# Kernel optimization log

Measured on AMD Instinct MI355X. Metric: run time of the kernel, lower is better.

Reference implementation:

```python
import jax, jax.numpy as jnp
import numpy as np

B, T, D, H = 2, 2048, 1024, 16
HD = D // H  # head_dim = 64


def setup_inputs() -> dict:
    key = jax.random.key(0)
    ks = jax.random.split(key, 5)
    s = 0.02
    return {
        "x": jax.random.normal(ks[0], (B, T, D), dtype=jnp.float32),
        "Wqkv": jax.random.normal(ks[1], (3 * D, D), dtype=jnp.float32) * s,
        "bqkv": jax.random.normal(ks[2], (3 * D,), dtype=jnp.float32) * s,
        "Wproj": jax.random.normal(ks[3], (D, D), dtype=jnp.float32) * s,
        "bproj": jax.random.normal(ks[4], (D,), dtype=jnp.float32) * s,
    }


def reference(x, Wqkv, bqkv, Wproj, bproj):
    b, t, d = x.shape
    qkv = x @ Wqkv.T + bqkv                      # [B,T,3D]
    q, k, v = jnp.split(qkv, 3, axis=-1)
    # [B,T,D] -> [B,H,T,HD]
    def to_heads(u):
        return u.reshape(b, t, H, HD).transpose(0, 2, 1, 3)
    q, k, v = to_heads(q), to_heads(k), to_heads(v)
    scale = 1.0 / jnp.sqrt(jnp.float32(HD))
    attn = jnp.einsum("bhqd,bhkd->bhqk", q, k) * scale   # [B,H,T,T]
    causal = jnp.tril(jnp.ones((t, t), dtype=bool))
    attn = jnp.where(causal[None, None, :, :], attn, -jnp.inf)
    attn = jax.nn.softmax(attn, axis=-1)
    scores = jnp.einsum("bhqk,bhkd->bhqd", attn, v)       # [B,H,T,HD]
    scores = scores.transpose(0, 2, 1, 3).reshape(b, t, d)
    return scores @ Wproj.T + bproj
```

## Files before the change

### kernel.cpp

```cpp
#include <hip/hip_runtime.h>

typedef __bf16 bf16_8 __attribute__((ext_vector_type(8)));
typedef __bf16 bf16_4 __attribute__((ext_vector_type(4)));
typedef __bf16 bf16_2 __attribute__((ext_vector_type(2)));
typedef float  f32_4  __attribute__((ext_vector_type(4)));
typedef float  f32_16 __attribute__((ext_vector_type(16)));

typedef __attribute__((address_space(1))) const void* as1_cvp;
typedef __attribute__((address_space(3))) void*       as3_vp;

__device__ __forceinline__ void load16_to_lds(const void* g, void* l) {
    __builtin_amdgcn_global_load_lds((as1_cvp)g, (as3_vp)l, 16, 0, 0);
}

__device__ __forceinline__ float fast_exp2(float x) {
#if __has_builtin(__builtin_amdgcn_exp2f)
    return __builtin_amdgcn_exp2f(x);
#else
    return exp2f(x);
#endif
}

__device__ __forceinline__ unsigned pk2(float lo, float hi) {
    union { bf16_2 h; unsigned u; } t;
    t.h = bf16_2{(__bf16)lo, (__bf16)hi};
    return t.u;
}

__device__ __forceinline__ void pswap(unsigned &a, unsigned &b) {
    asm("v_permlane32_swap_b32 %0, %1" : "+v"(a), "+v"(b));
}

__global__ __launch_bounds__(256) void cvt_all(
    const float* __restrict__ a, const float* __restrict__ b,
    const float* __restrict__ c, __bf16* __restrict__ out,
    int na4, int nb4, int nc4)
{
    int i = blockIdx.x * 256 + threadIdx.x;
    if (i >= na4 + nb4 + nc4) return;
    float4 f;
    if (i < na4)            f = ((const float4*)a)[i];
    else if (i < na4 + nb4) f = ((const float4*)b)[i - na4];
    else                    f = ((const float4*)c)[i - na4 - nb4];
    bf16_4 v = { (__bf16)f.x, (__bf16)f.y, (__bf16)f.z, (__bf16)f.w };
    ((bf16_4*)out)[i] = v;
}

#define BM 128

template<int OUT_BF16, int BN_, int QKV>
__global__ __launch_bounds__(256) void gemm_bt(
    const __bf16* __restrict__ A,
    const __bf16* __restrict__ B,
    const float*  __restrict__ bias,
    __bf16* __restrict__ Cb, float* __restrict__ Cf,
    __bf16* __restrict__ Vtb,
    int M, int N, int K, int ldc)
{
    constexpr int NT   = BN_ / 32;
    constexpr int CSTR = BN_ + (OUT_BF16 ? 8 : 4);
    __shared__ __align__(16) char smem[35840];
    __bf16* As = (__bf16*)smem;
    __bf16* Bs = As + 128 * 64;

    const int tid  = threadIdx.x;
    const int wave = tid >> 6;
    const int lane = tid & 63;
    const int wm = wave >> 1, wn = wave & 1;
    const int quad = lane >> 4, l16 = lane & 15;
    const int bm = blockIdx.y * BM, bn = blockIdx.x * BN_;

    const int r0 = tid >> 3;
    const int ch = tid & 7;
    const int cs = (ch ^ (r0 & 7)) * 8;

    f32_4 acc[4][NT];
    #pragma unroll
    for (int i = 0; i < 4; ++i)
        #pragma unroll
        for (int j = 0; j < NT; ++j)
            acc[i][j] = f32_4{0.f, 0.f, 0.f, 0.f};

    for (int k0 = 0; k0 < K; k0 += 64) {
        __syncthreads();
        #pragma unroll
        for (int p = 0; p < 4; ++p) {
            int row = p * 32 + r0;
            load16_to_lds(A + (size_t)(bm + row) * K + k0 + cs,
                          &As[(p * 32 + wave * 8) * 64]);
        }
        #pragma unroll
        for (int p = 0; p < BN_ / 32; ++p) {
            int row = p * 32 + r0;
            load16_to_lds(B + (size_t)(bn + row) * K + k0 + cs,
                          &Bs[(p * 32 + wave * 8) * 64]);
        }
        __syncthreads();

        #pragma unroll
        for (int h = 0; h < 2; ++h) {
            const int sl = ((quad + h * 4) ^ (l16 & 7)) * 8;
            bf16_8 af[4], bfr[NT];
            #pragma unroll
            for (int mt = 0; mt < 4; ++mt)
                af[mt] = *(const bf16_8*)&As[(wm * 64 + mt * 16 + l16) * 64 + sl];
            #pragma unroll
            for (int nt = 0; nt < NT; ++nt)
                bfr[nt] = *(const bf16_8*)&Bs[(wn * (BN_/2) + nt * 16 + l16) * 64 + sl];
            #pragma unroll
            for (int mt = 0; mt < 4; ++mt)
                #pragma unroll
                for (int nt = 0; nt < NT; ++nt)
                    acc[mt][nt] = __builtin_amdgcn_mfma_f32_16x16x32_bf16(
                        af[mt], bfr[nt], acc[mt][nt], 0, 0, 0);
        }
    }

    if (QKV && bn >= 2048) {
        const int b_ = bm >> 11;
        const int t0 = (bm & 2047) + wm * 64;
        #pragma unroll
        for (int nt = 0; nt < NT; ++nt) {
            int vrow = (bn - 2048) + wn * (BN_/2) + nt * 16 + l16;
            float bv = bias ? bias[2048 + vrow] : 0.f;
            #pragma unroll
            for (int mt = 0; mt < 4; ++mt) {
                bf16_4 ov;
                #pragma unroll
                for (int r = 0; r < 4; ++r)
                    ov[r] = (__bf16)(acc[mt][nt][r] + bv);
                *(bf16_4*)(Vtb + ((size_t)b_ * 1024 + vrow) * 2048
                           + t0 + mt * 16 + quad * 4) = ov;
            }
        }
        return;
    }

    __syncthreads();

    if (OUT_BF16) {
        __bf16* Cs = (__bf16*)smem;
        #pragma unroll
        for (int mt = 0; mt < 4; ++mt)
            #pragma unroll
            for (int nt = 0; nt < NT; ++nt) {
                int col = wn * (BN_/2) + nt * 16 + l16;
                float bv = bias ? bias[bn + col] : 0.f;
                #pragma unroll
                for (int r = 0; r < 4; ++r)
                    Cs[(wm * 64 + mt * 16 + quad * 4 + r) * CSTR + col] =
                        (__bf16)(acc[mt][nt][r] + bv);
            }
        __syncthreads();
        const int rr = tid >> 4, cc = (tid & 15) * 8;
        #pragma unroll
        for (int p = 0; p < 8; ++p) {
            int row = p * 16 + rr;
            bf16_8 v = *(const bf16_8*)&Cs[row * CSTR + cc];
            *(bf16_8*)(Cb + (size_t)(bm + row) * ldc + bn + cc) = v;
        }
    } else {
        float* Cs = (float*)smem;
        #pragma unroll
        for (int mt = 0; mt < 4; ++mt)
            #pragma unroll
            for (int nt = 0; nt < NT; ++nt) {
                int col = wn * (BN_/2) + nt * 16 + l16;
                float bv = bias ? bias[bn + col] : 0.f;
                #pragma unroll
                for (int r = 0; r < 4; ++r)
                    Cs[(wm * 64 + mt * 16 + quad * 4 + r) * CSTR + col] =
                        acc[mt][nt][r] + bv;
            }
        __syncthreads();
        const int rr = tid >> 4, cc = (tid & 15) * 4;
        #pragma unroll
        for (int p = 0; p < 8; ++p) {
            int row = p * 16 + rr;
            float4 v = *(const float4*)&Cs[row * CSTR + cc];
            *(float4*)(Cf + (size_t)(bm + row) * ldc + bn + cc) = v;
        }
    }
}

__global__ __launch_bounds__(256, 2) void attn_kernel(
    const __bf16* __restrict__ qk, const __bf16* __restrict__ vt,
    __bf16* __restrict__ out)
{
    constexpr int T = 2048;
    __shared__ __align__(16) char pool[49152];
    __bf16* Ks = (__bf16*)pool;
    __bf16* Vt = (__bf16*)(pool + 24576);
    float*  Om = (float*)pool;
    float*  Lm = (float*)(pool + 34816);

    const int tid  = threadIdx.x;
    const int wave = tid >> 6;
    const int lane = tid & 63;
    const int wq = wave & 1, wg = wave >> 1;
    const int l32 = lane & 31, hh = lane >> 5;

    const int fid  = blockIdx.x;
    const int xcd  = fid & 7;
    const int hsel = fid >> 8;
    const int w    = (fid >> 3) & 31;
    const int qt   = hsel ? (7 - (w >> 2)) : ((w >> 2) + 8);
    const int bh   = xcd * 4 + (w & 3);
    const int b = bh >> 4, h = bh & 15;
    const int jmax = 2 * qt + 1;

    const size_t rowbase = (size_t)b * T;
    const __bf16* Kbase = qk + 1024 + h * 64;
    const __bf16* Vbase = vt + (size_t)bh * 64 * 2048;

    const int sr   = tid >> 3;
    const int schf = (tid & 7) ^ (sr & 7);

    constexpr float QSCALE = 0.125f * 1.4426950408889634f;
    bf16_8 aq[2][4];
    #pragma unroll
    for (int qq = 0; qq < 2; ++qq)
        #pragma unroll
        for (int df = 0; df < 4; ++df) {
            const __bf16* qp = qk + (rowbase + qt*128 + wq*64 + qq*32 + l32)*2048
                               + h*64 + df*16 + hh*8;
            bf16_8 v = *(const bf16_8*)qp;
            #pragma unroll
            for (int u = 0; u < 8; ++u) v[u] = (__bf16)((float)v[u] * QSCALE);
            aq[qq][df] = v;
        }

    #pragma unroll
    for (int t0 = 0; t0 < 2; ++t0)
        #pragma unroll
        for (int p = 0; p < 2; ++p) {
            load16_to_lds(Kbase + (rowbase + t0*64 + sr + 32*p)*2048 + schf*8,
                          Ks + t0*4096 + p*2048 + wave*512);
            load16_to_lds(Vbase + (size_t)(sr + 32*p)*2048 + t0*64 + schf*8,
                          Vt + t0*4096 + p*2048 + wave*512);
        }

    f32_16 O[2][2];
    #pragma unroll
    for (int dt = 0; dt < 2; ++dt)
        #pragma unroll
        for (int qq = 0; qq < 2; ++qq)
            #pragma unroll
            for (int r = 0; r < 16; ++r) O[dt][qq][r] = 0.f;
    float l_i[2] = {0.f, 0.f};

    int cur = 0;
    int sb  = 2;
    for (int j = 0; j <= jmax; ++j) {
        if (j < jmax) asm volatile("s_waitcnt vmcnt(4)" ::: "memory");
        else          asm volatile("s_waitcnt vmcnt(0)" ::: "memory");
        __builtin_amdgcn_s_barrier();

        const int jn = j + 2;
        if (jn <= jmax) {
            #pragma unroll
            for (int p = 0; p < 2; ++p) {
                load16_to_lds(Kbase + (rowbase + jn*64 + sr + 32*p)*2048 + schf*8,
                              Ks + sb*4096 + p*2048 + wave*512);
                load16_to_lds(Vbase + (size_t)(sr + 32*p)*2048 + jn*64 + schf*8,
                              Vt + sb*4096 + p*2048 + wave*512);
            }
        }

        const int krow = wg*32 + l32;
        const int ksw  = krow & 7;
        f32_16 S[2];
        __builtin_amdgcn_s_setprio(1);
        bf16_8 kf[4];
        #pragma unroll
        for (int df = 0; df < 4; ++df)
            kf[df] = *(const bf16_8*)&Ks[cur*4096 + krow*64 + (((2*df + hh) ^ ksw) << 3)];
        #pragma unroll
        for (int qq = 0; qq < 2; ++qq) {
            f32_16 z;
            #pragma unroll
            for (int r = 0; r < 16; ++r) z[r] = 0.f;
            #pragma unroll
            for (int df = 0; df < 4; ++df)
                z = __builtin_amdgcn_mfma_f32_32x32x16_bf16(kf[df], aq[qq][df], z, 0, 0, 0);
            S[qq] = z;
        }
        __builtin_amdgcn_s_setprio(0);

        const bool diag = (j >= 2*qt);
        unsigned fr[2][8];
        #pragma unroll
        for (int qq = 0; qq < 2; ++qq) {
            float pe[16];
            const int qg = qt*128 + wq*64 + qq*32 + l32;
            #pragma unroll
            for (int r = 0; r < 16; ++r) {
                float e = fast_exp2(S[qq][r]);
                if (diag) {
                    int key = j*64 + wg*32 + (r&3) + 8*(r>>2) + 4*hh;
                    if (key > qg) e = 0.f;
                }
                pe[r] = e;
                l_i[qq] += e;
            }
            unsigned A = pk2(pe[0],  pe[1]),  Bv = pk2(pe[2],  pe[3]),
                     C = pk2(pe[4],  pe[5]),  D  = pk2(pe[6],  pe[7]),
                     E = pk2(pe[8],  pe[9]),  F  = pk2(pe[10], pe[11]),
                     G = pk2(pe[12], pe[13]), H  = pk2(pe[14], pe[15]);
            pswap(A, C); pswap(Bv, D); pswap(E, G); pswap(F, H);
            fr[qq][0] = A; fr[qq][1] = Bv; fr[qq][2] = C; fr[qq][3] = D;
            fr[qq][4] = E; fr[qq][5] = F;  fr[qq][6] = G; fr[qq][7] = H;
        }

        __builtin_amdgcn_s_setprio(1);
        #pragma unroll
        for (int kh = 0; kh < 2; ++kh) {
            #pragma unroll
            for (int dt = 0; dt < 2; ++dt) {
                const int d = dt*32 + l32;
                bf16_8 vf = *(const bf16_8*)&Vt[cur*4096 + d*64 +
                                (((wg*4 + kh*2 + hh) ^ (d & 7)) << 3)];
                #pragma unroll
                for (int qq = 0; qq < 2; ++qq) {
                    union { unsigned dw[4]; bf16_8 v; } u;
                    u.dw[0] = fr[qq][kh*4+0]; u.dw[1] = fr[qq][kh*4+1];
                    u.dw[2] = fr[qq][kh*4+2]; u.dw[3] = fr[qq][kh*4+3];
                    O[dt][qq] = __builtin_amdgcn_mfma_f32_32x32x16_bf16(
                        vf, u.v, O[dt][qq], 0, 0, 0);
                }
            }
        }
        __builtin_amdgcn_s_setprio(0);

        cur = (cur == 2) ? 0 : cur + 1;
        sb  = (sb  == 2) ? 0 : sb  + 1;
    }

    float lw[2];
    #pragma unroll
    for (int qq = 0; qq < 2; ++qq) {
        float v = l_i[qq];
        v += __shfl_xor(v, 32, 64);
        lw[qq] = v;
    }

    __syncthreads();
    if (wg == 1) {
        #pragma unroll
        for (int qq = 0; qq < 2; ++qq) {
            const int qrow = wq*64 + qq*32 + l32;
            #pragma unroll
            for (int dt = 0; dt < 2; ++dt)
                #pragma unroll
                for (int g = 0; g < 4; ++g) {
                    f32_4 t = { O[dt][qq][g*4+0], O[dt][qq][g*4+1],
                                O[dt][qq][g*4+2], O[dt][qq][g*4+3] };
                    *(f32_4*)&Om[qrow*68 + dt*32 + g*8 + hh*4] = t;
                }
            if (hh == 0) Lm[qrow] = lw[qq];
        }
    }
    __syncthreads();
    if (wg == 0) {
        #pragma unroll
        for (int qq = 0; qq < 2; ++qq) {
            const int qrow = wq*64 + qq*32 + l32;
            const float inv = 1.f / (lw[qq] + Lm[qrow]);
            const size_t obase = (rowbase + qt*128 + qrow) * 1024 + h*64;
            #pragma unroll
            for (int dt = 0; dt < 2; ++dt)
                #pragma unroll
                for (int g = 0; g < 4; ++g) {
                    f32_4 o2 = *(const f32_4*)&Om[qrow*68 + dt*32 + g*8 + hh*4];
                    bf16_4 ov;
                    #pragma unroll
                    for (int r = 0; r < 4; ++r)
                        ov[r] = (__bf16)((O[dt][qq][g*4+r] + o2[r]) * inv);
                    *(bf16_4*)(out + obase + dt*32 + g*8 + hh*4) = ov;
                }
        }
    }
}

extern "C" void kernel_launch(void* const* d_in, const int* in_sizes, int n_in,
                              void* d_out, int out_size, void* d_ws, size_t ws_size,
                              hipStream_t stream)
{
    constexpr int Bc = 2, Tc = 2048, Dc = 1024;
    constexpr int M  = Bc * Tc;
    constexpr int N1 = 3 * Dc;

    const float* x     = (const float*)d_in[0];
    const float* Wqkv  = (const float*)d_in[1];
    const float* bqkv  = (const float*)d_in[2];
    const float* Wproj = (const float*)d_in[3];
    const float* bproj = (const float*)d_in[4];
    float* outp = (float*)d_out;

    __bf16* xb     = (__bf16*)d_ws;
    __bf16* wqkvb  = xb     + (size_t)M * Dc;
    __bf16* wprojb = wqkvb  + (size_t)N1 * Dc;
    __bf16* qkb    = wprojb + (size_t)Dc * Dc;
    __bf16* vtb    = qkb    + (size_t)M * 2048;
    __bf16* attnb  = vtb    + (size_t)Bc * 1024 * 2048;

    {
        int na4 = M * Dc / 4, nb4 = N1 * Dc / 4, nc4 = Dc * Dc / 4;
        int n4 = na4 + nb4 + nc4;
        cvt_all<<<(n4 + 255) / 256, 256, 0, stream>>>(x, Wqkv, Wproj, xb, na4, nb4, nc4);
    }

    gemm_bt<1, 128, 1><<<dim3(N1 / 128, M / BM), 256, 0, stream>>>(
        xb, wqkvb, bqkv, qkb, nullptr, vtb, M, N1, Dc, 2048);

    attn_kernel<<<dim3(512), 256, 0, stream>>>(qkb, vtb, attnb);

    gemm_bt<0, 64, 0><<<dim3(Dc / 64, M / BM), 256, 0, stream>>>(
        attnb, wprojb, bproj, nullptr, outp, nullptr, M, Dc, Dc, Dc);
}
```

Measured before the change: 164.0 us.

## Add triple-buffered LDS prefetch pipeline to output projection GEMM

Adds a PIPE template variant of the bf16 GEMM that keeps three LDS stages and issues global-to-LDS loads two k-steps ahead. It uses explicit vmcnt waits with a single barrier per iteration, so memory latency can overlap with MFMA work. Only the output projection GEMM (BN=64) uses it. The cost is 3x LDS per block, about 72KB with BN=64, which may reduce occupancy. Correctness relies on the hand-counted vmcnt(6) matching the 6 loads issued per stage per thread.

```diff
diff --git a/kernel.cpp b/kernel.cpp
--- a/kernel.cpp
+++ b/kernel.cpp
@@ -48,7 +48,7 @@
 
 #define BM 128
 
-template<int OUT_BF16, int BN_, int QKV>
+template<int OUT_BF16, int BN_, int QKV, int PIPE>
 __global__ __launch_bounds__(256) void gemm_bt(
     const __bf16* __restrict__ A,
     const __bf16* __restrict__ B,
@@ -59,9 +59,9 @@
 {
     constexpr int NT   = BN_ / 32;
     constexpr int CSTR = BN_ + (OUT_BF16 ? 8 : 4);
-    __shared__ __align__(16) char smem[35840];
-    __bf16* As = (__bf16*)smem;
-    __bf16* Bs = As + 128 * 64;
+    constexpr int BUFB = (128 * 64 + BN_ * 64) * 2;
+    constexpr int SMEMSZ = PIPE ? (3 * BUFB) : 35840;
+    __shared__ __align__(16) char smem[SMEMSZ];
 
     const int tid  = threadIdx.x;
     const int wave = tid >> 6;
@@ -81,38 +81,99 @@
         for (int j = 0; j < NT; ++j)
             acc[i][j] = f32_4{0.f, 0.f, 0.f, 0.f};
 
-    for (int k0 = 0; k0 < K; k0 += 64) {
-        __syncthreads();
-        #pragma unroll
-        for (int p = 0; p < 4; ++p) {
-            int row = p * 32 + r0;
-            load16_to_lds(A + (size_t)(bm + row) * K + k0 + cs,
-                          &As[(p * 32 + wave * 8) * 64]);
-        }
-        #pragma unroll
-        for (int p = 0; p < BN_ / 32; ++p) {
-            int row = p * 32 + r0;
-            load16_to_lds(B + (size_t)(bn + row) * K + k0 + cs,
-                          &Bs[(p * 32 + wave * 8) * 64]);
-        }
-        __syncthreads();
-
-        #pragma unroll
-        for (int h = 0; h < 2; ++h) {
-            const int sl = ((quad + h * 4) ^ (l16 & 7)) * 8;
-            bf16_8 af[4], bfr[NT];
-            #pragma unroll
-            for (int mt = 0; mt < 4; ++mt)
-                af[mt] = *(const bf16_8*)&As[(wm * 64 + mt * 16 + l16) * 64 + sl];
-            #pragma unroll
-            for (int nt = 0; nt < NT; ++nt)
-                bfr[nt] = *(const bf16_8*)&Bs[(wn * (BN_/2) + nt * 16 + l16) * 64 + sl];
-            #pragma unroll
-            for (int mt = 0; mt < 4; ++mt)
+    if constexpr (!PIPE) {
+        __bf16* As = (__bf16*)smem;
+        __bf16* Bs = As + 128 * 64;
+        for (int k0 = 0; k0 < K; k0 += 64) {
+            __syncthreads();
+            #pragma unroll
+            for (int p = 0; p < 4; ++p) {
+                int row = p * 32 + r0;
+                load16_to_lds(A + (size_t)(bm + row) * K + k0 + cs,
+                              &As[(p * 32 + wave * 8) * 64]);
+            }
+            #pragma unroll
+            for (int p = 0; p < BN_ / 32; ++p) {
+                int row = p * 32 + r0;
+                load16_to_lds(B + (size_t)(bn + row) * K + k0 + cs,
+                              &Bs[(p * 32 + wave * 8) * 64]);
+            }
+            __syncthreads();
+
+            #pragma unroll
+            for (int h = 0; h < 2; ++h) {
+                const int sl = ((quad + h * 4) ^ (l16 & 7)) * 8;
+                bf16_8 af[4], bfr[NT];
+                #pragma unroll
+                for (int mt = 0; mt < 4; ++mt)
+                    af[mt] = *(const bf16_8*)&As[(wm * 64 + mt * 16 + l16) * 64 + sl];
                 #pragma unroll
                 for (int nt = 0; nt < NT; ++nt)
-                    acc[mt][nt] = __builtin_amdgcn_mfma_f32_16x16x32_bf16(
-                        af[mt], bfr[nt], acc[mt][nt], 0, 0, 0);
+                    bfr[nt] = *(const bf16_8*)&Bs[(wn * (BN_/2) + nt * 16 + l16) * 64 + sl];
+                #pragma unroll
+                for (int mt = 0; mt < 4; ++mt)
+                    #pragma unroll
+                    for (int nt = 0; nt < NT; ++nt)
+                        acc[mt][nt] = __builtin_amdgcn_mfma_f32_16x16x32_bf16(
+                            af[mt], bfr[nt], acc[mt][nt], 0, 0, 0);
+            }
+        }
+    } else {
+        const int nit = K / 64;
+        #pragma unroll
+        for (int t = 0; t < 2; ++t) {
+            __bf16* AsT = (__bf16*)(smem + t * BUFB);
+            __bf16* BsT = AsT + 128 * 64;
+            #pragma unroll
+            for (int p = 0; p < 4; ++p)
+                load16_to_lds(A + (size_t)(bm + p * 32 + r0) * K + t * 64 + cs,
+                              &AsT[(p * 32 + wave * 8) * 64]);
+            #pragma unroll
+            for (int p = 0; p < BN_ / 32; ++p)
+                load16_to_lds(B + (size_t)(bn + p * 32 + r0) * K + t * 64 + cs,
+                              &BsT[(p * 32 + wave * 8) * 64]);
+        }
+        int cur = 0, sb = 2;
+        for (int j = 0; j < nit; ++j) {
+            if (j < nit - 1) asm volatile("s_waitcnt vmcnt(6)" ::: "memory");
+            else             asm volatile("s_waitcnt vmcnt(0)" ::: "memory");
+            __builtin_amdgcn_s_barrier();
+
+            if (j + 2 < nit) {
+                const int k0 = (j + 2) * 64;
+                __bf16* AsT = (__bf16*)(smem + sb * BUFB);
+                __bf16* BsT = AsT + 128 * 64;
+                #pragma unroll
+                for (int p = 0; p < 4; ++p)
+                    load16_to_lds(A + (size_t)(bm + p * 32 + r0) * K + k0 + cs,
+                                  &AsT[(p * 32 + wave * 8) * 64]);
+                #pragma unroll
+                for (int p = 0; p < BN_ / 32; ++p)
+                    load16_to_lds(B + (size_t)(bn + p * 32 + r0) * K + k0 + cs,
+                                  &BsT[(p * 32 + wave * 8) * 64]);
+            }
+
+            __bf16* As = (__bf16*)(smem + cur * BUFB);
+            __bf16* Bs = As + 128 * 64;
+            #pragma unroll
+            for (int h = 0; h < 2; ++h) {
+                const int sl = ((quad + h * 4) ^ (l16 & 7)) * 8;
+                bf16_8 af[4], bfr[NT];
+                #pragma unroll
+                for (int mt = 0; mt < 4; ++mt)
+                    af[mt] = *(const bf16_8*)&As[(wm * 64 + mt * 16 + l16) * 64 + sl];
+                #pragma unroll
+                for (int nt = 0; nt < NT; ++nt)
+                    bfr[nt] = *(const bf16_8*)&Bs[(wn * (BN_/2) + nt * 16 + l16) * 64 + sl];
+                #pragma unroll
+                for (int mt = 0; mt < 4; ++mt)
+                    #pragma unroll
+                    for (int nt = 0; nt < NT; ++nt)
+                        acc[mt][nt] = __builtin_amdgcn_mfma_f32_16x16x32_bf16(
+                            af[mt], bfr[nt], acc[mt][nt], 0, 0, 0);
+            }
+            cur = (cur == 2) ? 0 : cur + 1;
+            sb  = (sb  == 2) ? 0 : sb  + 1;
         }
     }
 
@@ -410,11 +471,11 @@
         cvt_all<<<(n4 + 255) / 256, 256, 0, stream>>>(x, Wqkv, Wproj, xb, na4, nb4, nc4);
     }
 
-    gemm_bt<1, 128, 1><<<dim3(N1 / 128, M / BM), 256, 0, stream>>>(
+    gemm_bt<1, 128, 1, 0><<<dim3(N1 / 128, M / BM), 256, 0, stream>>>(
         xb, wqkvb, bqkv, qkb, nullptr, vtb, M, N1, Dc, 2048);
 
     attn_kernel<<<dim3(512), 256, 0, stream>>>(qkb, vtb, attnb);
 
-    gemm_bt<0, 64, 0><<<dim3(Dc / 64, M / BM), 256, 0, stream>>>(
+    gemm_bt<0, 64, 0, 1><<<dim3(Dc / 64, M / BM), 256, 0, stream>>>(
         attnb, wprojb, bproj, nullptr, outp, nullptr, M, Dc, Dc, Dc);
 }
```

New measurement: 162.8 us. Within noise of the previous version (-0.7%).
